# Kernel tuning notes

Hardware: AMD Instinct MI355X
Metric: run time of the kernel (lower is better)

The kernel has to match this reference:

```python
import jax, jax.numpy as jnp
import numpy as np

N_SUB = 262144      # total subgraphs (rows of h_subgraph)
NUM_GRAPHS = 8192   # graphs in batch
D = 128             # channel width
L = 3               # number of fc / fc_sum layers
NUM_TASKS = 10


def segment_mean(x, idx, num_segments):
    # scatter_mean: sum per segment, divide by count (count>=1 guard like torch_scatter)
    sums = jax.ops.segment_sum(x, idx, num_segments=num_segments)
    cnt = jax.ops.segment_sum(jnp.ones((x.shape[0],), dtype=x.dtype), idx, num_segments=num_segments)
    return sums / jnp.maximum(cnt, 1.0)[:, None]


def setup_inputs() -> dict:
    key = jax.random.key(0)
    ks = jax.random.split(key, 10)
    s = 1.0 / np.sqrt(D)
    h_subgraph = jax.random.normal(ks[0], (N_SUB, D), dtype=jnp.float32)
    subgraph_idx = jnp.sort(jax.random.randint(ks[1], (N_SUB,), 0, NUM_GRAPHS, dtype=jnp.int32))
    W_fc = jax.random.normal(ks[2], (L, D, D), dtype=jnp.float32) * s
    b_fc = jax.random.normal(ks[3], (L, D), dtype=jnp.float32) * s
    W_sum = jax.random.normal(ks[4], (L, D, D), dtype=jnp.float32) * s
    b_sum = jax.random.normal(ks[5], (L, D), dtype=jnp.float32) * s
    W_f1 = jax.random.normal(ks[6], (D, 2 * D), dtype=jnp.float32) * s
    b_f1 = jax.random.normal(ks[7], (2 * D,), dtype=jnp.float32) * s
    W_f2 = jax.random.normal(ks[8], (2 * D, NUM_TASKS), dtype=jnp.float32) / np.sqrt(2 * D)
    b_f2 = jax.random.normal(ks[9], (NUM_TASKS,), dtype=jnp.float32) / np.sqrt(2 * D)
    return {"h_subgraph": h_subgraph, "subgraph_idx": subgraph_idx,
            "W_fc": W_fc, "b_fc": b_fc, "W_sum": W_sum, "b_sum": b_sum,
            "W_f1": W_f1, "b_f1": b_f1, "W_f2": W_f2, "b_f2": b_f2}


def reference(h_subgraph, subgraph_idx, W_fc, b_fc, W_sum, b_sum, W_f1, b_f1, W_f2, b_f2):
    h = h_subgraph
    # non-invariant branch: per-layer Linear + scatter_mean + Linear + gather + ELU
    for i in range(L):
        x1 = h @ W_fc[i] + b_fc[i]                                  # [N, D]
        g = segment_mean(h, subgraph_idx, NUM_GRAPHS)               # [G, D]
        x2 = g @ W_sum[i] + b_sum[i]                                # [G, D]
        h = jax.nn.elu(x1 + x2[subgraph_idx])                       # gather + combine
    h_graph = segment_mean(h, subgraph_idx, NUM_GRAPHS)             # [G, D]
    # final MLP head
    out = jax.nn.relu(h_graph @ W_f1 + b_f1) @ W_f2 + b_f2          # [G, num_tasks]
    return out
```

## Files before the change

### kernel.cpp

```cpp
#include <hip/hip_runtime.h>

#define NSUB 262144
#define NG   8192
#define DIM  128
#define NT   10

typedef __attribute__((ext_vector_type(4))) float f32x4;
typedef __attribute__((ext_vector_type(8))) short short8;
typedef unsigned short ushort_t;
typedef unsigned int uint_t;

__device__ __forceinline__ float bf2f(ushort_t u){
    union { uint_t i; float f; } v; v.i = ((uint_t)u) << 16; return v.f;
}
__device__ __forceinline__ ushort_t f2bf(float f){
    union { __bf16 b; ushort_t u; } v; v.b = (__bf16)f; return v.u;
}


__global__ __launch_bounds__(256) void prep_kernel(const float* __restrict__ Wfc,
                                                   ushort_t* __restrict__ Wt,
                                                   float* __restrict__ g,
                                                   float* __restrict__ cnt)
{
    const int b = blockIdx.x;
    if (b < 2056){
        const long t = (long)b * 256 + threadIdx.x;
        const f32x4 z = {0.f, 0.f, 0.f, 0.f};
        if (t < 524288) ((f32x4*)g)[t] = z;
        else            ((f32x4*)cnt)[t - 524288] = z;
    } else {
        int t = (b - 2056) * 256 + threadIdx.x;
        int i   = t >> 11;
        int rem = t & 2047;
        int ks  = rem >> 9;
        int f   = (rem >> 6) & 7;
        int l   = rem & 63;
        int c   = f * 16 + (l & 15);
        int kb  = ks * 32 + (l >> 4) * 8;
        short8 v;
        #pragma unroll
        for (int j = 0; j < 8; j++)
            v[j] = (short)f2bf(Wfc[i * 16384 + (kb + j) * 128 + c]);
        *(short8*)(Wt + (long)t * 8) = v;
    }
}

__global__ __launch_bounds__(256) void seg0_kernel(const float* __restrict__ h0,
                                                   const int* __restrict__ idx,
                                                   float* __restrict__ gsum,
                                                   float* __restrict__ cnt)
{
    __shared__ int sidx[128];
    const int tid = threadIdx.x;
    const int bid = ((blockIdx.x & 7) << 8) | (blockIdx.x >> 3);
    const long base = (long)bid * 128;
    if (tid < 128) sidx[tid] = idx[base + tid];
    __syncthreads();

    const int cg = tid & 31, ch = tid >> 5;
    const int rloc0 = ch * 16;
    f32x4 acc = {0.f, 0.f, 0.f, 0.f};
    int cur = sidx[rloc0], n = 0;
    #pragma unroll
    for (int j = 0; j < 16; j++){
        const int g = sidx[rloc0 + j];
        if (g != cur){
            float* gp = gsum + (long)cur * 128 + cg * 4;
            atomicAdd(gp + 0, acc[0]); atomicAdd(gp + 1, acc[1]);
            atomicAdd(gp + 2, acc[2]); atomicAdd(gp + 3, acc[3]);
            if (cg == 0) atomicAdd(cnt + cur, (float)n);
            acc = {0.f, 0.f, 0.f, 0.f}; n = 0; cur = g;
        }
        f32x4 v = *(const f32x4*)(h0 + (base + rloc0 + j) * 128 + cg * 4);
        acc += v; n++;
    }
    float* gp = gsum + (long)cur * 128 + cg * 4;
    atomicAdd(gp + 0, acc[0]); atomicAdd(gp + 1, acc[1]);
    atomicAdd(gp + 2, acc[2]); atomicAdd(gp + 3, acc[3]);
    if (cg == 0) atomicAdd(cnt + cur, (float)n);
}

__global__ __launch_bounds__(256) void x2_kernel(float* g,
                                                 const float* __restrict__ cnt,
                                                 const float* __restrict__ Wsum,
                                                 const float* __restrict__ bsum,
                                                 const float* __restrict__ bfc,
                                                 float* __restrict__ x2)
{
    __shared__ float gm[16][128];
    __shared__ float invc[16];
    const int tid = threadIdx.x;
    const int r0 = blockIdx.x * 16;
    if (tid < 16) invc[tid] = 1.f / fmaxf(cnt[r0 + tid], 1.f);
    __syncthreads();
    #pragma unroll
    for (int p = 0; p < 8; p++){
        int e = tid + p * 256;
        int row = e >> 7, col = e & 127;
        float val = g[(long)(r0 + row) * 128 + col];
        gm[row][col] = val * invc[row];
        g[(long)(r0 + row) * 128 + col] = 0.f;
    }
    __syncthreads();
    const int c = tid & 127, rh = tid >> 7;
    float acc[8];
    #pragma unroll
    for (int i = 0; i < 8; i++) acc[i] = bsum[c] + bfc[c];
    for (int k = 0; k < 128; k++){
        float w = Wsum[k * 128 + c];
        #pragma unroll
        for (int i = 0; i < 8; i++) acc[i] += gm[rh * 8 + i][k] * w;
    }
    #pragma unroll
    for (int i = 0; i < 8; i++) x2[(long)(r0 + rh * 8 + i) * 128 + c] = acc[i];
}

template<int FIRST>
__global__ __launch_bounds__(256, 4) void layer_kernel(const void* __restrict__ hin_,
                                                    ushort_t* hout,
                                                    const ushort_t* __restrict__ Wt,
                                                    const float* __restrict__ x2,
                                                    const int* __restrict__ idx,
                                                    float* __restrict__ gnext)
{
    __shared__ __align__(16) ushort_t seg[128 * 132];
    __shared__ int sidx[128];
    const int tid = threadIdx.x;
    const int bid = ((blockIdx.x & 7) << 8) | (blockIdx.x >> 3);
    const long base = (long)bid * 128;

    const int wv = tid >> 6, ln = tid & 63;
    const int ln15 = ln & 15, grp = ln >> 4;
    const long Rbase = (long)bid * 8 + wv * 2;

    short8 b8[8];
    if (FIRST){
        const float* hp = (const float*)hin_;
        f32x4 hv[16];
        #pragma unroll
        for (int ks = 0; ks < 4; ks++)
            #pragma unroll
            for (int q = 0; q < 2; q++){
                const long r = (Rbase + q) * 16 + ln15;
                const float* p = hp + r * 128 + ks * 32 + grp * 8;
                hv[(ks * 2 + q) * 2 + 0] = *(const f32x4*)p;
                hv[(ks * 2 + q) * 2 + 1] = *(const f32x4*)(p + 4);
            }
        #pragma unroll
        for (int i = 0; i < 8; i++){
            short8 s;
            #pragma unroll
            for (int j = 0; j < 4; j++){
                s[j]     = (short)f2bf(hv[2 * i][j]);
                s[4 + j] = (short)f2bf(hv[2 * i + 1][j]);
            }
            b8[i] = s;
        }
    } else {
        const ushort_t* hp = (const ushort_t*)hin_;
        #pragma unroll
        for (int ks = 0; ks < 4; ks++)
            #pragma unroll
            for (int q = 0; q < 2; q++)
                b8[ks * 2 + q] = *(const short8*)(hp + (((Rbase + q) * 4 + ks) * 64 + ln) * 8);
    }

    if (tid < 128) sidx[tid] = idx[base + tid];

    f32x4 acc[2][8];
    #pragma unroll
    for (int q = 0; q < 2; q++)
        #pragma unroll
        for (int f = 0; f < 8; f++) acc[q][f] = {0.f, 0.f, 0.f, 0.f};

    __builtin_amdgcn_s_setprio(1);
    #pragma unroll
    for (int ks = 0; ks < 4; ks++){
        short8 a0[4], a1[4];
        #pragma unroll
        for (int f = 0; f < 4; f++)
            a0[f] = *(const short8*)(Wt + ((long)(ks * 8 + f) * 64 + ln) * 8);
        #pragma unroll
        for (int f = 0; f < 4; f++)
            #pragma unroll
            for (int q = 0; q < 2; q++)
                acc[q][f] = __builtin_amdgcn_mfma_f32_16x16x32_bf16(a0[f], b8[ks * 2 + q], acc[q][f], 0, 0, 0);
        #pragma unroll
        for (int f = 0; f < 4; f++)
            a1[f] = *(const short8*)(Wt + ((long)(ks * 8 + 4 + f) * 64 + ln) * 8);
        #pragma unroll
        for (int f = 0; f < 4; f++)
            #pragma unroll
            for (int q = 0; q < 2; q++)
                acc[q][4 + f] = __builtin_amdgcn_mfma_f32_16x16x32_bf16(a1[f], b8[ks * 2 + q], acc[q][4 + f], 0, 0, 0);
    }
    __builtin_amdgcn_s_setprio(0);

    #pragma unroll
    for (int q = 0; q < 2; q++){
        const int lr = wv * 32 + q * 16 + ln15;
        const int g = idx[base + lr];
        const float* x2r = x2 + (long)g * 128;
        f32x4 xv[8];
        #pragma unroll
        for (int f = 0; f < 8; f++)
            xv[f] = *(const f32x4*)(x2r + f * 16 + grp * 4);
        #pragma unroll
        for (int f = 0; f < 8; f++){
            const int cb = f * 16 + grp * 4;
            ushort_t h4[4];
            #pragma unroll
            for (int i = 0; i < 4; i++){
                float v = acc[q][f][i] + xv[f][i];
                v = v > 0.f ? v : (__expf(v) - 1.f);
                h4[i] = f2bf(v);
            }
            uint2 pk;
            pk.x = (uint_t)h4[0] | ((uint_t)h4[1] << 16);
            pk.y = (uint_t)h4[2] | ((uint_t)h4[3] << 16);
            const long c16 = ((Rbase + q) * 4 + (f >> 1)) * 64
                           + (2 * (f & 1) + (grp >> 1)) * 16 + ln15;
            *(uint2*)((char*)hout + c16 * 16 + (grp & 1) * 8) = pk;
            *(uint2*)((char*)seg + lr * 264 + cb * 2) = pk;
        }
    }
    __syncthreads();

    const int c = tid & 63, ch2 = tid >> 6;
    const int rr0 = ch2 * 32;
    float a0 = 0.f, a1 = 0.f;
    int cur = sidx[rr0];
    for (int j = 0; j < 32; j++){
        const int rr = rr0 + j;
        const int g = sidx[rr];
        if (g != cur){
            atomicAdd(gnext + (long)cur * 128 + 2 * c,     a0);
            atomicAdd(gnext + (long)cur * 128 + 2 * c + 1, a1);
            a0 = a1 = 0.f; cur = g;
        }
        uint_t u = *(const uint_t*)((const char*)seg + rr * 264 + c * 4);
        a0 += bf2f((ushort_t)(u & 0xffff));
        a1 += bf2f((ushort_t)(u >> 16));
    }
    atomicAdd(gnext + (long)cur * 128 + 2 * c,     a0);
    atomicAdd(gnext + (long)cur * 128 + 2 * c + 1, a1);
}

__global__ __launch_bounds__(256) void head_kernel(const float* __restrict__ g,
                                                   const float* __restrict__ cnt,
                                                   const float* __restrict__ Wf1,
                                                   const float* __restrict__ bf1,
                                                   const float* __restrict__ Wf2,
                                                   const float* __restrict__ bf2,
                                                   float* __restrict__ out)
{
    __shared__ float hm[8][128];
    __shared__ float t1[8][256];
    __shared__ float invc[8];
    const int tid = threadIdx.x;
    const int r0 = blockIdx.x * 8;
    if (tid < 8) invc[tid] = 1.f / fmaxf(cnt[r0 + tid], 1.f);
    __syncthreads();
    #pragma unroll
    for (int p = 0; p < 4; p++){
        int e = tid + p * 256;
        int row = e >> 7, col = e & 127;
        hm[row][col] = g[(long)(r0 + row) * 128 + col] * invc[row];
    }
    __syncthreads();
    {
        const int c = tid;
        float acc[8];
        #pragma unroll
        for (int r = 0; r < 8; r++) acc[r] = bf1[c];
        for (int k = 0; k < 128; k++){
            float w = Wf1[k * 256 + c];
            #pragma unroll
            for (int r = 0; r < 8; r++) acc[r] += hm[r][k] * w;
        }
        #pragma unroll
        for (int r = 0; r < 8; r++) t1[r][c] = fmaxf(acc[r], 0.f);
    }
    __syncthreads();
    if (tid < 80){
        const int r = tid / 10, c = tid % 10;
        float acc = bf2[c];
        for (int k = 0; k < 256; k++) acc += t1[r][k] * Wf2[k * 10 + c];
        out[(long)(r0 + r) * 10 + c] = acc;
    }
}

extern "C" void kernel_launch(void* const* d_in, const int* in_sizes, int n_in,
                              void* d_out, int out_size, void* d_ws, size_t ws_size,
                              hipStream_t stream)
{
    const float* h0   = (const float*)d_in[0];
    const int*   idx  = (const int*)d_in[1];
    const float* Wfc  = (const float*)d_in[2];
    const float* bfc  = (const float*)d_in[3];
    const float* Wsum = (const float*)d_in[4];
    const float* bsum = (const float*)d_in[5];
    const float* Wf1  = (const float*)d_in[6];
    const float* bf1  = (const float*)d_in[7];
    const float* Wf2  = (const float*)d_in[8];
    const float* bf2  = (const float*)d_in[9];
    float* out = (float*)d_out;

    char* ws = (char*)d_ws;
    ushort_t* hbuf = (ushort_t*)ws;
    float* g0  = (float*)(ws + 67108864);
    float* g1  = (float*)(ws + 71303168);
    float* x2  = (float*)(ws + 75497472);
    float* cnt = (float*)(ws + 79691776);
    ushort_t* Wt = (ushort_t*)(ws + 79724544);
    if (ws_size < 79822848ull) return;

    prep_kernel<<<2080, 256, 0, stream>>>(Wfc, Wt, g0, cnt);

    seg0_kernel<<<NSUB / 128, 256, 0, stream>>>(h0, idx, g0, cnt);
    x2_kernel<<<NG / 16, 256, 0, stream>>>(g0, cnt, Wsum, bsum, bfc, x2);
    layer_kernel<1><<<NSUB / 128, 256, 0, stream>>>(h0, hbuf, Wt, x2, idx, g1);

    x2_kernel<<<NG / 16, 256, 0, stream>>>(g1, cnt, Wsum + 16384, bsum + 128, bfc + 128, x2);
    layer_kernel<0><<<NSUB / 128, 256, 0, stream>>>(hbuf, hbuf, Wt + 16384, x2, idx, g0);

    x2_kernel<<<NG / 16, 256, 0, stream>>>(g0, cnt, Wsum + 32768, bsum + 256, bfc + 256, x2);
    layer_kernel<0><<<NSUB / 128, 256, 0, stream>>>(hbuf, hbuf, Wt + 32768, x2, idx, g1);

    head_kernel<<<NG / 8, 256, 0, stream>>>(g1, cnt, Wf1, bf1, Wf2, bf2, out);
}
```

Measured before the change: 245.5 us.

## Process two 128-row tiles per block and skip final h writeback

Each layer block now handles 256 rows as two 128-row halves. The block loads both halves' inputs up front, then for each half runs the MFMA GEMM, ELU and segment reduction one after the other, with the grid halved to match. The goal is to put the second half's global loads in flight under the first half's compute. A new NOWRITE template flag drops the bf16 h store in the last layer, since only its segment sums are used downstream. The x2 gather is also interleaved per fragment instead of preloaded. Holding both halves' inputs raises register pressure, which may spill or cut occupancy under launch_bounds(256,4), and fewer blocks reduces parallelism.

```diff
diff --git a/kernel.cpp b/kernel.cpp
--- a/kernel.cpp
+++ b/kernel.cpp
@@ -116,7 +116,7 @@
     for (int i = 0; i < 8; i++) x2[(long)(r0 + rh * 8 + i) * 128 + c] = acc[i];
 }
 
-template<int FIRST>
+template<int FIRST, int NOWRITE>
 __global__ __launch_bounds__(256, 4) void layer_kernel(const void* __restrict__ hin_,
                                                     ushort_t* hout,
                                                     const ushort_t* __restrict__ Wt,
@@ -125,126 +125,234 @@
                                                     float* __restrict__ gnext)
 {
     __shared__ __align__(16) ushort_t seg[128 * 132];
-    __shared__ int sidx[128];
+    __shared__ int sidx[256];
     const int tid = threadIdx.x;
-    const int bid = ((blockIdx.x & 7) << 8) | (blockIdx.x >> 3);
-    const long base = (long)bid * 128;
+    const int bid = ((blockIdx.x & 7) << 7) | (blockIdx.x >> 3);
+    const long base = (long)bid * 256;
 
     const int wv = tid >> 6, ln = tid & 63;
     const int ln15 = ln & 15, grp = ln >> 4;
-    const long Rbase = (long)bid * 8 + wv * 2;
-
-    short8 b8[8];
+    const long Rb0 = (long)bid * 16 + wv * 2;
+    const long Rb1 = Rb0 + 8;
+
+    short8 b8a[8], b8b[8];
     if (FIRST){
         const float* hp = (const float*)hin_;
-        f32x4 hv[16];
-        #pragma unroll
-        for (int ks = 0; ks < 4; ks++)
-            #pragma unroll
-            for (int q = 0; q < 2; q++){
-                const long r = (Rbase + q) * 16 + ln15;
+        #pragma unroll
+        for (int half = 0; half < 2; half++){
+            f32x4 hv[8];
+            #pragma unroll
+            for (int e = 0; e < 4; e++){
+                const int i = half * 4 + e;
+                const int ks = i >> 1, q = i & 1;
+                const long r = (Rb0 + q) * 16 + ln15;
                 const float* p = hp + r * 128 + ks * 32 + grp * 8;
-                hv[(ks * 2 + q) * 2 + 0] = *(const f32x4*)p;
-                hv[(ks * 2 + q) * 2 + 1] = *(const f32x4*)(p + 4);
-            }
-        #pragma unroll
-        for (int i = 0; i < 8; i++){
-            short8 s;
-            #pragma unroll
-            for (int j = 0; j < 4; j++){
-                s[j]     = (short)f2bf(hv[2 * i][j]);
-                s[4 + j] = (short)f2bf(hv[2 * i + 1][j]);
-            }
-            b8[i] = s;
+                hv[e * 2 + 0] = *(const f32x4*)p;
+                hv[e * 2 + 1] = *(const f32x4*)(p + 4);
+            }
+            #pragma unroll
+            for (int e = 0; e < 4; e++){
+                short8 s;
+                #pragma unroll
+                for (int j = 0; j < 4; j++){
+                    s[j]     = (short)f2bf(hv[e * 2][j]);
+                    s[4 + j] = (short)f2bf(hv[e * 2 + 1][j]);
+                }
+                b8a[half * 4 + e] = s;
+            }
+        }
+        #pragma unroll
+        for (int half = 0; half < 2; half++){
+            f32x4 hv[8];
+            #pragma unroll
+            for (int e = 0; e < 4; e++){
+                const int i = half * 4 + e;
+                const int ks = i >> 1, q = i & 1;
+                const long r = (Rb1 + q) * 16 + ln15;
+                const float* p = hp + r * 128 + ks * 32 + grp * 8;
+                hv[e * 2 + 0] = *(const f32x4*)p;
+                hv[e * 2 + 1] = *(const f32x4*)(p + 4);
+            }
+            #pragma unroll
+            for (int e = 0; e < 4; e++){
+                short8 s;
+                #pragma unroll
+                for (int j = 0; j < 4; j++){
+                    s[j]     = (short)f2bf(hv[e * 2][j]);
+                    s[4 + j] = (short)f2bf(hv[e * 2 + 1][j]);
+                }
+                b8b[half * 4 + e] = s;
+            }
         }
     } else {
         const ushort_t* hp = (const ushort_t*)hin_;
         #pragma unroll
         for (int ks = 0; ks < 4; ks++)
             #pragma unroll
-            for (int q = 0; q < 2; q++)
-                b8[ks * 2 + q] = *(const short8*)(hp + (((Rbase + q) * 4 + ks) * 64 + ln) * 8);
-    }
-
-    if (tid < 128) sidx[tid] = idx[base + tid];
-
-    f32x4 acc[2][8];
-    #pragma unroll
-    for (int q = 0; q < 2; q++)
-        #pragma unroll
-        for (int f = 0; f < 8; f++) acc[q][f] = {0.f, 0.f, 0.f, 0.f};
-
-    __builtin_amdgcn_s_setprio(1);
-    #pragma unroll
-    for (int ks = 0; ks < 4; ks++){
-        short8 a0[4], a1[4];
-        #pragma unroll
-        for (int f = 0; f < 4; f++)
-            a0[f] = *(const short8*)(Wt + ((long)(ks * 8 + f) * 64 + ln) * 8);
-        #pragma unroll
-        for (int f = 0; f < 4; f++)
-            #pragma unroll
-            for (int q = 0; q < 2; q++)
-                acc[q][f] = __builtin_amdgcn_mfma_f32_16x16x32_bf16(a0[f], b8[ks * 2 + q], acc[q][f], 0, 0, 0);
-        #pragma unroll
-        for (int f = 0; f < 4; f++)
-            a1[f] = *(const short8*)(Wt + ((long)(ks * 8 + 4 + f) * 64 + ln) * 8);
-        #pragma unroll
-        for (int f = 0; f < 4; f++)
-            #pragma unroll
-            for (int q = 0; q < 2; q++)
-                acc[q][4 + f] = __builtin_amdgcn_mfma_f32_16x16x32_bf16(a1[f], b8[ks * 2 + q], acc[q][4 + f], 0, 0, 0);
-    }
-    __builtin_amdgcn_s_setprio(0);
-
-    #pragma unroll
-    for (int q = 0; q < 2; q++){
-        const int lr = wv * 32 + q * 16 + ln15;
-        const int g = idx[base + lr];
-        const float* x2r = x2 + (long)g * 128;
-        f32x4 xv[8];
-        #pragma unroll
-        for (int f = 0; f < 8; f++)
-            xv[f] = *(const f32x4*)(x2r + f * 16 + grp * 4);
-        #pragma unroll
-        for (int f = 0; f < 8; f++){
-            const int cb = f * 16 + grp * 4;
-            ushort_t h4[4];
-            #pragma unroll
-            for (int i = 0; i < 4; i++){
-                float v = acc[q][f][i] + xv[f][i];
-                v = v > 0.f ? v : (__expf(v) - 1.f);
-                h4[i] = f2bf(v);
-            }
-            uint2 pk;
-            pk.x = (uint_t)h4[0] | ((uint_t)h4[1] << 16);
-            pk.y = (uint_t)h4[2] | ((uint_t)h4[3] << 16);
-            const long c16 = ((Rbase + q) * 4 + (f >> 1)) * 64
-                           + (2 * (f & 1) + (grp >> 1)) * 16 + ln15;
-            *(uint2*)((char*)hout + c16 * 16 + (grp & 1) * 8) = pk;
-            *(uint2*)((char*)seg + lr * 264 + cb * 2) = pk;
-        }
-    }
-    __syncthreads();
-
-    const int c = tid & 63, ch2 = tid >> 6;
-    const int rr0 = ch2 * 32;
-    float a0 = 0.f, a1 = 0.f;
-    int cur = sidx[rr0];
-    for (int j = 0; j < 32; j++){
-        const int rr = rr0 + j;
-        const int g = sidx[rr];
-        if (g != cur){
-            atomicAdd(gnext + (long)cur * 128 + 2 * c,     a0);
-            atomicAdd(gnext + (long)cur * 128 + 2 * c + 1, a1);
-            a0 = a1 = 0.f; cur = g;
-        }
-        uint_t u = *(const uint_t*)((const char*)seg + rr * 264 + c * 4);
-        a0 += bf2f((ushort_t)(u & 0xffff));
-        a1 += bf2f((ushort_t)(u >> 16));
-    }
-    atomicAdd(gnext + (long)cur * 128 + 2 * c,     a0);
-    atomicAdd(gnext + (long)cur * 128 + 2 * c + 1, a1);
+            for (int q = 0; q < 2; q++){
+                b8a[ks * 2 + q] = *(const short8*)(hp + (((Rb0 + q) * 4 + ks) * 64 + ln) * 8);
+                b8b[ks * 2 + q] = *(const short8*)(hp + (((Rb1 + q) * 4 + ks) * 64 + ln) * 8);
+            }
+    }
+
+    if (tid < 256) sidx[tid] = idx[base + tid];
+
+    {
+        f32x4 acc[2][8];
+        #pragma unroll
+        for (int q = 0; q < 2; q++)
+            #pragma unroll
+            for (int f = 0; f < 8; f++) acc[q][f] = {0.f, 0.f, 0.f, 0.f};
+
+        __builtin_amdgcn_s_setprio(1);
+        #pragma unroll
+        for (int ks = 0; ks < 4; ks++){
+            short8 a0[4], a1[4];
+            #pragma unroll
+            for (int f = 0; f < 4; f++)
+                a0[f] = *(const short8*)(Wt + ((long)(ks * 8 + f) * 64 + ln) * 8);
+            #pragma unroll
+            for (int f = 0; f < 4; f++)
+                #pragma unroll
+                for (int q = 0; q < 2; q++)
+                    acc[q][f] = __builtin_amdgcn_mfma_f32_16x16x32_bf16(a0[f], b8a[ks * 2 + q], acc[q][f], 0, 0, 0);
+            #pragma unroll
+            for (int f = 0; f < 4; f++)
+                a1[f] = *(const short8*)(Wt + ((long)(ks * 8 + 4 + f) * 64 + ln) * 8);
+            #pragma unroll
+            for (int f = 0; f < 4; f++)
+                #pragma unroll
+                for (int q = 0; q < 2; q++)
+                    acc[q][4 + f] = __builtin_amdgcn_mfma_f32_16x16x32_bf16(a1[f], b8a[ks * 2 + q], acc[q][4 + f], 0, 0, 0);
+        }
+        __builtin_amdgcn_s_setprio(0);
+
+        #pragma unroll
+        for (int q = 0; q < 2; q++){
+            const int lr = wv * 32 + q * 16 + ln15;
+            const int g = idx[base + lr];
+            const float* x2r = x2 + (long)g * 128;
+            #pragma unroll
+            for (int f = 0; f < 8; f++){
+                const int cb = f * 16 + grp * 4;
+                f32x4 xv = *(const f32x4*)(x2r + cb);
+                ushort_t h4[4];
+                #pragma unroll
+                for (int i = 0; i < 4; i++){
+                    float v = acc[q][f][i] + xv[i];
+                    v = v > 0.f ? v : (__expf(v) - 1.f);
+                    h4[i] = f2bf(v);
+                }
+                uint2 pk;
+                pk.x = (uint_t)h4[0] | ((uint_t)h4[1] << 16);
+                pk.y = (uint_t)h4[2] | ((uint_t)h4[3] << 16);
+                const long c16 = ((Rb0 + q) * 4 + (f >> 1)) * 64
+                               + (2 * (f & 1) + (grp >> 1)) * 16 + ln15;
+                if (!NOWRITE) *(uint2*)((char*)hout + c16 * 16 + (grp & 1) * 8) = pk;
+                *(uint2*)((char*)seg + lr * 264 + cb * 2) = pk;
+            }
+        }
+    }
+    __syncthreads();
+    {
+        const int c = tid & 63, ch2 = tid >> 6;
+        const int rr0 = ch2 * 32;
+        float a0 = 0.f, a1 = 0.f;
+        int cur = sidx[rr0];
+        for (int j = 0; j < 32; j++){
+            const int lr = rr0 + j;
+            const int g = sidx[lr];
+            if (g != cur){
+                atomicAdd(gnext + (long)cur * 128 + 2 * c,     a0);
+                atomicAdd(gnext + (long)cur * 128 + 2 * c + 1, a1);
+                a0 = a1 = 0.f; cur = g;
+            }
+            uint_t u = *(const uint_t*)((const char*)seg + lr * 264 + c * 4);
+            a0 += bf2f((ushort_t)(u & 0xffff));
+            a1 += bf2f((ushort_t)(u >> 16));
+        }
+        atomicAdd(gnext + (long)cur * 128 + 2 * c,     a0);
+        atomicAdd(gnext + (long)cur * 128 + 2 * c + 1, a1);
+    }
+    __syncthreads();
+
+    {
+        f32x4 acc[2][8];
+        #pragma unroll
+        for (int q = 0; q < 2; q++)
+            #pragma unroll
+            for (int f = 0; f < 8; f++) acc[q][f] = {0.f, 0.f, 0.f, 0.f};
+
+        __builtin_amdgcn_s_setprio(1);
+        #pragma unroll
+        for (int ks = 0; ks < 4; ks++){
+            short8 a0[4], a1[4];
+            #pragma unroll
+            for (int f = 0; f < 4; f++)
+                a0[f] = *(const short8*)(Wt + ((long)(ks * 8 + f) * 64 + ln) * 8);
+            #pragma unroll
+            for (int f = 0; f < 4; f++)
+                #pragma unroll
+                for (int q = 0; q < 2; q++)
+                    acc[q][f] = __builtin_amdgcn_mfma_f32_16x16x32_bf16(a0[f], b8b[ks * 2 + q], acc[q][f], 0, 0, 0);
+            #pragma unroll
+            for (int f = 0; f < 4; f++)
+                a1[f] = *(const short8*)(Wt + ((long)(ks * 8 + 4 + f) * 64 + ln) * 8);
+            #pragma unroll
+            for (int f = 0; f < 4; f++)
+                #pragma unroll
+                for (int q = 0; q < 2; q++)
+                    acc[q][4 + f] = __builtin_amdgcn_mfma_f32_16x16x32_bf16(a1[f], b8b[ks * 2 + q], acc[q][4 + f], 0, 0, 0);
+        }
+        __builtin_amdgcn_s_setprio(0);
+
+        #pragma unroll
+        for (int q = 0; q < 2; q++){
+            const int lr = wv * 32 + q * 16 + ln15;
+            const int g = idx[base + 128 + lr];
+            const float* x2r = x2 + (long)g * 128;
+            #pragma unroll
+            for (int f = 0; f < 8; f++){
+                const int cb = f * 16 + grp * 4;
+                f32x4 xv = *(const f32x4*)(x2r + cb);
+                ushort_t h4[4];
+                #pragma unroll
+                for (int i = 0; i < 4; i++){
+                    float v = acc[q][f][i] + xv[i];
+                    v = v > 0.f ? v : (__expf(v) - 1.f);
+                    h4[i] = f2bf(v);
+                }
+                uint2 pk;
+                pk.x = (uint_t)h4[0] | ((uint_t)h4[1] << 16);
+                pk.y = (uint_t)h4[2] | ((uint_t)h4[3] << 16);
+                const long c16 = ((Rb1 + q) * 4 + (f >> 1)) * 64
+                               + (2 * (f & 1) + (grp >> 1)) * 16 + ln15;
+                if (!NOWRITE) *(uint2*)((char*)hout + c16 * 16 + (grp & 1) * 8) = pk;
+                *(uint2*)((char*)seg + lr * 264 + cb * 2) = pk;
+            }
+        }
+    }
+    __syncthreads();
+    {
+        const int c = tid & 63, ch2 = tid >> 6;
+        const int rr0 = ch2 * 32;
+        float a0 = 0.f, a1 = 0.f;
+        int cur = sidx[128 + rr0];
+        for (int j = 0; j < 32; j++){
+            const int lr = rr0 + j;
+            const int g = sidx[128 + lr];
+            if (g != cur){
+                atomicAdd(gnext + (long)cur * 128 + 2 * c,     a0);
+                atomicAdd(gnext + (long)cur * 128 + 2 * c + 1, a1);
+                a0 = a1 = 0.f; cur = g;
+            }
+            uint_t u = *(const uint_t*)((const char*)seg + lr * 264 + c * 4);
+            a0 += bf2f((ushort_t)(u & 0xffff));
+            a1 += bf2f((ushort_t)(u >> 16));
+        }
+        atomicAdd(gnext + (long)cur * 128 + 2 * c,     a0);
+        atomicAdd(gnext + (long)cur * 128 + 2 * c + 1, a1);
+    }
 }
 
 __global__ __launch_bounds__(256) void head_kernel(const float* __restrict__ g,
@@ -320,13 +428,13 @@
 
     seg0_kernel<<<NSUB / 128, 256, 0, stream>>>(h0, idx, g0, cnt);
     x2_kernel<<<NG / 16, 256, 0, stream>>>(g0, cnt, Wsum, bsum, bfc, x2);
-    layer_kernel<1><<<NSUB / 128, 256, 0, stream>>>(h0, hbuf, Wt, x2, idx, g1);
+    layer_kernel<1, 0><<<NSUB / 256, 256, 0, stream>>>(h0, hbuf, Wt, x2, idx, g1);
 
     x2_kernel<<<NG / 16, 256, 0, stream>>>(g1, cnt, Wsum + 16384, bsum + 128, bfc + 128, x2);
-    layer_kernel<0><<<NSUB / 128, 256, 0, stream>>>(hbuf, hbuf, Wt + 16384, x2, idx, g0);
+    layer_kernel<0, 0><<<NSUB / 256, 256, 0, stream>>>(hbuf, hbuf, Wt + 16384, x2, idx, g0);
 
     x2_kernel<<<NG / 16, 256, 0, stream>>>(g0, cnt, Wsum + 32768, bsum + 256, bfc + 256, x2);
-    layer_kernel<0><<<NSUB / 128, 256, 0, stream>>>(hbuf, hbuf, Wt + 32768, x2, idx, g1);
+    layer_kernel<0, 1><<<NSUB / 256, 256, 0, stream>>>(hbuf, hbuf, Wt + 32768, x2, idx, g1);
 
     head_kernel<<<NG / 8, 256, 0, stream>>>(g1, cnt, Wf1, bf1, Wf2, bf2, out);
 }
```

Result: slower. 377.7 us (+53.9%).
